# Performance work log

Hardware: AMD Instinct MI355X
Metric: run time of the kernel (lower is better)

Reference implementation:

```python
import jax, jax.numpy as jnp
import numpy as np

N_NODES = 50000
N_EDGES = 800000
IN_DIM, HID_DIM, OUT_DIM = 128, 64, 64
NEG_SLOPE = 0.2


def setup_inputs() -> dict:
    key = jax.random.key(0)
    ks = jax.random.split(key, 9)
    return {
        "x": jax.random.normal(ks[0], (N_NODES, IN_DIM), dtype=jnp.float32),
        "edge_index": jax.random.randint(ks[1], (2, N_EDGES), 0, N_NODES, dtype=jnp.int64),
        "W1": jax.random.normal(ks[2], (IN_DIM, HID_DIM), dtype=jnp.float32) * 0.1,
        "a1_src": jax.random.normal(ks[3], (HID_DIM,), dtype=jnp.float32) * 0.1,
        "a1_dst": jax.random.normal(ks[4], (HID_DIM,), dtype=jnp.float32) * 0.1,
        "b1": jnp.zeros((HID_DIM,), dtype=jnp.float32),
        "W2": jax.random.normal(ks[5], (HID_DIM, OUT_DIM), dtype=jnp.float32) * 0.1,
        "a2_src": jax.random.normal(ks[6], (OUT_DIM,), dtype=jnp.float32) * 0.1,
        "a2_dst": jax.random.normal(ks[7], (OUT_DIM,), dtype=jnp.float32) * 0.1,
        "b2": jnp.zeros((OUT_DIM,), dtype=jnp.float32),
    }


def gat_conv(x, src, dst, W, a_src, a_dst, b, n_nodes):
    """Single-head GATConv (PyG semantics, self-loops already appended)."""
    h = x @ W                               # [N, D]
    s_src = h @ a_src                       # [N]
    s_dst = h @ a_dst                       # [N]
    e = s_src[src] + s_dst[dst]             # [E] edge logits
    e = jnp.where(e >= 0, e, NEG_SLOPE * e)  # leaky_relu(0.2)
    # softmax over incoming edges of each destination node (numerically stable)
    m = jax.ops.segment_max(e, dst, num_segments=n_nodes)   # [N]
    e = jnp.exp(e - m[dst])
    denom = jax.ops.segment_sum(e, dst, num_segments=n_nodes)
    alpha = e / denom[dst]                  # [E]
    out = jax.ops.segment_sum(alpha[:, None] * h[src], dst, num_segments=n_nodes)
    return out + b


def reference(x, edge_index, W1, a1_src, a1_dst, b1, W2, a2_src, a2_dst, b2):
    n = x.shape[0]
    loop = jnp.arange(n, dtype=edge_index.dtype)
    src = jnp.concatenate([edge_index[0], loop])  # add self loops (PyG default)
    dst = jnp.concatenate([edge_index[1], loop])
    h = jax.nn.relu(gat_conv(x, src, dst, W1, a1_src, a1_dst, b1, n))
    out = gat_conv(h, src, dst, W2, a2_src, a2_dst, b2, n)
    return out
```

## Files before the change

### kernel.cpp

```cpp
#include <hip/hip_runtime.h>
#include <hip/hip_fp16.h>

#define N_NODES 50000
#define N_EDGES 800000
#define NEG_SLOPE 0.2f
#define NBKT 196
#define EBLK 200
#define CHUNK 4000

__device__ __forceinline__ float leaky(float x) { return x >= 0.f ? x : NEG_SLOPE * x; }
__device__ __forceinline__ float readlane_f(float v, int i) {
    return __uint_as_float(__builtin_amdgcn_readlane(__float_as_uint(v), i));
}
__device__ __forceinline__ unsigned enc_f(float f) {
    unsigned u = __float_as_uint(f);
    return (int)u < 0 ? ~u : (u | 0x80000000u);
}
__device__ __forceinline__ float dec_f(unsigned e) {
    return __uint_as_float((int)e < 0 ? (e & 0x7FFFFFFFu) : ~e);
}

template <int K>
__global__ __launch_bounds__(256) void gat_gemm_kernel(
    const float* __restrict__ x, const float* __restrict__ W,
    const float* __restrict__ a_src, const float* __restrict__ a_dst,
    __half* __restrict__ h, float* __restrict__ s_src, float* __restrict__ s_dst,
    unsigned* __restrict__ gmax_enc, int n)
{
    constexpr int BK = 32;
    __shared__ float Wl[BK][64];
    __shared__ float xt[BK][68];
    __shared__ float asl[64], adl[64];
    __shared__ float wm[4];

    int tid = threadIdx.x;
    if (tid < 64) { asl[tid] = a_src[tid]; adl[tid] = a_dst[tid]; }
    int tx = tid & 15, ty = tid >> 4;
    int row0 = blockIdx.x * 64;

    float acc[4][4] = {};

    for (int k0 = 0; k0 < K; k0 += BK) {
        __syncthreads();
        {
            const float4* Wg = (const float4*)&W[(size_t)k0 * 64];
            float4* Ws = (float4*)&Wl[0][0];
            Ws[tid]       = Wg[tid];
            Ws[tid + 256] = Wg[tid + 256];
        }
        #pragma unroll
        for (int it = 0; it < 2; ++it) {
            int idx = tid + it * 256;
            int r = idx >> 3, kq = idx & 7;
            int grow = row0 + r;
            float4 v = (grow < n) ? *(const float4*)&x[(size_t)grow * K + k0 + kq * 4]
                                  : make_float4(0.f, 0.f, 0.f, 0.f);
            xt[kq * 4 + 0][r] = v.x;
            xt[kq * 4 + 1][r] = v.y;
            xt[kq * 4 + 2][r] = v.z;
            xt[kq * 4 + 3][r] = v.w;
        }
        __syncthreads();

        #pragma unroll
        for (int kk = 0; kk < BK; ++kk) {
            float4 wv = *(const float4*)&Wl[kk][tx * 4];
            float4 xv = *(const float4*)&xt[kk][ty * 4];
            acc[0][0] += xv.x * wv.x; acc[0][1] += xv.x * wv.y; acc[0][2] += xv.x * wv.z; acc[0][3] += xv.x * wv.w;
            acc[1][0] += xv.y * wv.x; acc[1][1] += xv.y * wv.y; acc[1][2] += xv.y * wv.z; acc[1][3] += xv.y * wv.w;
            acc[2][0] += xv.z * wv.x; acc[2][1] += xv.z * wv.y; acc[2][2] += xv.z * wv.z; acc[2][3] += xv.z * wv.w;
            acc[3][0] += xv.w * wv.x; acc[3][1] += xv.w * wv.y; acc[3][2] += xv.w * wv.z; acc[3][3] += xv.w * wv.w;
        }
    }

    float wmax = -INFINITY;
    #pragma unroll
    for (int i = 0; i < 4; ++i) {
        int grow = row0 + ty * 4 + i;
        if (grow < n) {
            __half2 p0 = __floats2half2_rn(acc[i][0], acc[i][1]);
            __half2 p1 = __floats2half2_rn(acc[i][2], acc[i][3]);
            uint2 pk = make_uint2(*(unsigned*)&p0, *(unsigned*)&p1);
            *(uint2*)&h[(size_t)grow * 64 + tx * 4] = pk;
        }
        float s1 = acc[i][0] * asl[tx*4+0] + acc[i][1] * asl[tx*4+1]
                 + acc[i][2] * asl[tx*4+2] + acc[i][3] * asl[tx*4+3];
        float s2 = acc[i][0] * adl[tx*4+0] + acc[i][1] * adl[tx*4+1]
                 + acc[i][2] * adl[tx*4+2] + acc[i][3] * adl[tx*4+3];
        #pragma unroll
        for (int m = 1; m < 16; m <<= 1) {
            s1 += __shfl_xor(s1, m, 64);
            s2 += __shfl_xor(s2, m, 64);
        }
        if (grow < n) wmax = fmaxf(wmax, s1);
        if (tx == 0 && grow < n) { s_src[grow] = s1; s_dst[grow] = s2; }
    }
    wmax = fmaxf(wmax, __shfl_xor(wmax, 16, 64));
    wmax = fmaxf(wmax, __shfl_xor(wmax, 32, 64));
    if ((tid & 63) == 0) wm[tid >> 6] = wmax;
    __syncthreads();
    if (tid == 0) {
        float bm = fmaxf(fmaxf(wm[0], wm[1]), fmaxf(wm[2], wm[3]));
        atomicMax(gmax_enc, enc_f(bm));
    }
}

__global__ __launch_bounds__(256) void p1_count(
    const int* __restrict__ dst, int* __restrict__ cnt, unsigned* __restrict__ gmaxu)
{
    __shared__ int bins[NBKT];
    int tid = threadIdx.x, b = blockIdx.x;
    if (tid < NBKT) bins[tid] = 0;
    if (b == 0 && tid >= 254) gmaxu[tid - 254] = 0;
    __syncthreads();
    int e0 = b * CHUNK;
    for (int e = e0 + tid; e < e0 + CHUNK; e += 256)
        atomicAdd(&bins[dst[e] >> 8], 1);
    __syncthreads();
    if (tid < NBKT) cnt[b * NBKT + tid] = bins[tid];
}

__global__ __launch_bounds__(256) void p2_scan(
    int* __restrict__ cnt, int* __restrict__ btot)
{
    __shared__ int tmp[256];
    int j = blockIdx.x, tid = threadIdx.x;
    int v = (tid < EBLK) ? cnt[tid * NBKT + j] : 0;
    tmp[tid] = v; __syncthreads();
    for (int off = 1; off < 256; off <<= 1) {
        int a = (tid >= off) ? tmp[tid - off] : 0;
        __syncthreads();
        tmp[tid] += a;
        __syncthreads();
    }
    if (tid < EBLK) cnt[tid * NBKT + j] = tmp[tid] - v;
    if (tid == EBLK - 1) btot[j] = tmp[tid];
}

__global__ __launch_bounds__(256) void p3_bucket(
    const int* __restrict__ src, const int* __restrict__ dst,
    const int* __restrict__ cnt, const int* __restrict__ btot,
    unsigned* __restrict__ bkted)
{
    __shared__ int tmp[256];
    __shared__ int boffL[NBKT];
    int b = blockIdx.x, tid = threadIdx.x;
    int v = (tid < NBKT) ? btot[tid] : 0;
    tmp[tid] = v; __syncthreads();
    for (int off = 1; off < 256; off <<= 1) {
        int a = (tid >= off) ? tmp[tid - off] : 0;
        __syncthreads();
        tmp[tid] += a;
        __syncthreads();
    }
    if (tid < NBKT) boffL[tid] = (tmp[tid] - v) + cnt[b * NBKT + tid];
    __syncthreads();
    int e0 = b * CHUNK;
    for (int e = e0 + tid; e < e0 + CHUNK; e += 256) {
        int d = dst[e], s = src[e];
        int pos = atomicAdd(&boffL[d >> 8], 1);
        bkted[pos] = ((unsigned)(d & 255) << 16) | (unsigned)s;
    }
}

__global__ __launch_bounds__(256) void p4_csr(
    const unsigned* __restrict__ bkted, const int* __restrict__ btot,
    int* __restrict__ row_off, int* __restrict__ csr_src)
{
    __shared__ int tmp[256];
    __shared__ int cur[256];
    __shared__ int s_beg, s_end;
    int j = blockIdx.x, tid = threadIdx.x;
    int v = (tid < NBKT) ? btot[tid] : 0;
    tmp[tid] = v; __syncthreads();
    for (int off = 1; off < 256; off <<= 1) {
        int a = (tid >= off) ? tmp[tid - off] : 0;
        __syncthreads();
        tmp[tid] += a;
        __syncthreads();
    }
    if (tid == j) { s_beg = tmp[tid] - v; s_end = tmp[tid]; }
    cur[tid] = 0;
    __syncthreads();
    int beg = s_beg, end = s_end;

    for (int e = beg + tid; e < end; e += 256)
        atomicAdd(&cur[bkted[e] >> 16], 1);
    __syncthreads();
    int c = cur[tid];
    tmp[tid] = c; __syncthreads();
    for (int off = 1; off < 256; off <<= 1) {
        int a = (tid >= off) ? tmp[tid - off] : 0;
        __syncthreads();
        tmp[tid] += a;
        __syncthreads();
    }
    int offx = tmp[tid] - c;
    int node = j * 256 + tid;
    if (node < N_NODES) row_off[node] = beg + offx;
    if (node == 0) row_off[N_NODES] = N_EDGES;
    __syncthreads();
    cur[tid] = offx;
    __syncthreads();
    for (int e = beg + tid; e < end; e += 256) {
        unsigned u = bkted[e];
        int pos = beg + atomicAdd(&cur[u >> 16], 1);
        csr_src[pos] = (int)(u & 0xFFFFu);
    }
}

template <bool RELU>
__global__ __launch_bounds__(256) void gat_node_kernel(
    const int* __restrict__ row_off, const int* __restrict__ csr_src,
    const float* __restrict__ s_src, const float* __restrict__ s_dst,
    const __half* __restrict__ h, const float* __restrict__ b,
    const unsigned* __restrict__ gmax_enc, float* __restrict__ out, int n)
{
    int row = blockIdx.x * 4 + (threadIdx.x >> 6);
    int lane = threadIdx.x & 63;
    if (row >= n) return;

    int beg = row_off[row], end = row_off[row + 1];
    int deg = end - beg;
    float sd = s_dst[row];
    float m = leaky(dec_f(*gmax_enc) + sd);
    float s_self = s_src[row];
    float hself = __half2float(h[(size_t)row * 64 + lane]);
    float wself = __expf(leaky(s_self + sd) - m);

    if (deg <= 32) {
        int mysrc = row;
        if (lane < deg) mysrc = csr_src[beg + lane];
        float my_s = s_src[mysrc];
        float hv[32];
        #pragma unroll
        for (int j = 0; j < 32; ++j) {
            int s = __builtin_amdgcn_readlane(mysrc, j);
            hv[j] = __half2float(h[(size_t)s * 64 + lane]);
        }
        float mylogit = (lane < deg) ? leaky(my_s + sd) : -INFINITY;
        float w64 = __expf(mylogit - m);
        float den = w64;
        #pragma unroll
        for (int off = 32; off; off >>= 1)
            den += __shfl_xor(den, off, 64);
        den += wself;

        float acc = wself * hself;
        #pragma unroll
        for (int j = 0; j < 32; ++j)
            acc += readlane_f(w64, j) * hv[j];

        float v = acc / den + b[lane];
        if (RELU) v = fmaxf(v, 0.f);
        out[(size_t)row * 64 + lane] = v;
        return;
    }

    int   mysrc   = row;
    float mylogit = -INFINITY;
    if (lane < deg) {
        mysrc = csr_src[beg + lane];
        mylogit = leaky(s_src[mysrc] + sd);
    }
    float w64 = __expf(mylogit - m);
    float den = w64;
    #pragma unroll
    for (int off = 32; off; off >>= 1)
        den += __shfl_xor(den, off, 64);
    den += wself;

    float acc = wself * hself;
    int d0 = deg < 64 ? deg : 64;
    int nb = (d0 + 15) & ~15;
    for (int i = 0; i < nb; i += 16) {
        float hv[16];
        #pragma unroll
        for (int j = 0; j < 16; ++j) {
            int s = __builtin_amdgcn_readlane(mysrc, i + j);
            hv[j] = __half2float(h[(size_t)s * 64 + lane]);
        }
        #pragma unroll
        for (int j = 0; j < 16; ++j)
            acc += readlane_f(w64, i + j) * hv[j];
    }
    for (int e = beg + 64; e < end; ++e) {
        int s = csr_src[e];
        float w = __expf(leaky(s_src[s] + sd) - m);
        den += w;
        acc += w * __half2float(h[(size_t)s * 64 + lane]);
    }

    float v = acc / den + b[lane];
    if (RELU) v = fmaxf(v, 0.f);
    out[(size_t)row * 64 + lane] = v;
}

extern "C" void kernel_launch(void* const* d_in, const int* in_sizes, int n_in,
                              void* d_out, int out_size, void* d_ws, size_t ws_size,
                              hipStream_t stream) {
    const float* x   = (const float*)d_in[0];
    const int*   ei  = (const int*)d_in[1];
    const float* W1  = (const float*)d_in[2];
    const float* a1s = (const float*)d_in[3];
    const float* a1d = (const float*)d_in[4];
    const float* b1  = (const float*)d_in[5];
    const float* W2  = (const float*)d_in[6];
    const float* a2s = (const float*)d_in[7];
    const float* a2d = (const float*)d_in[8];
    const float* b2  = (const float*)d_in[9];
    float* out = (float*)d_out;

    const int* src = ei;
    const int* dst = ei + N_EDGES;

    char* p = (char*)d_ws;
    __half* h   = (__half*)p;           p += (size_t)N_NODES * 64 * 2;
    float* ssrc = (float*)p;            p += (size_t)N_NODES * 4;
    float* sdst = (float*)p;            p += (size_t)N_NODES * 4;
    int* row_off = (int*)p;             p += (size_t)(N_NODES + 1) * 4;
    unsigned* gmaxu = (unsigned*)p;     p += 4 * 4;
    int* csr_src = (int*)p;             p += (size_t)N_EDGES * 4;
    int* cnt     = (int*)p;             p += (size_t)EBLK * NBKT * 4;
    int* btot    = (int*)p;             p += (size_t)NBKT * 4;

    unsigned* bkted = (unsigned*)h;

    dim3 blk(256);
    int gemm_blocks = (N_NODES + 63) / 64;
    int node_blocks = (N_NODES + 3) / 4;

    p1_count<<<EBLK, blk, 0, stream>>>(dst, cnt, gmaxu);
    p2_scan<<<NBKT, blk, 0, stream>>>(cnt, btot);
    p3_bucket<<<EBLK, blk, 0, stream>>>(src, dst, cnt, btot, bkted);
    p4_csr<<<NBKT, blk, 0, stream>>>(bkted, btot, row_off, csr_src);

    gat_gemm_kernel<128><<<gemm_blocks, blk, 0, stream>>>(x, W1, a1s, a1d, h, ssrc, sdst, gmaxu + 0, N_NODES);
    gat_node_kernel<true><<<node_blocks, blk, 0, stream>>>(row_off, csr_src, ssrc, sdst, h, b1, gmaxu + 0, out, N_NODES);

    gat_gemm_kernel<64><<<gemm_blocks, blk, 0, stream>>>(out, W2, a2s, a2d, h, ssrc, sdst, gmaxu + 1, N_NODES);
    gat_node_kernel<false><<<node_blocks, blk, 0, stream>>>(row_off, csr_src, ssrc, sdst, h, b2, gmaxu + 1, out, N_NODES);
}
```

Baseline: 132.2 us.

## Split features into half planes, fuse GEMM with edge counting, two-edge gather per wave

Stores the fp16 projected features as two 32-column planes and runs the aggregation kernel once per plane. Each half-wave handles alternate edges, and the two halves are combined with a shuffle. The first GEMM is fused with the edge-count pass into one launch, writing per-block maxima that the scan kernel reduces, and the bucket buffer gets its own workspace. The smaller per-plane working set should fit the gathered data better in cache, at the cost of extra node-kernel launches and re-reading the CSR and scores for each plane. The small-degree fast path is removed, and nontemporal loads and stores are used for the CSR reads and output writes.

```diff
diff --git a/kernel.cpp b/kernel.cpp
--- a/kernel.cpp
+++ b/kernel.cpp
@@ -7,6 +7,7 @@
 #define NBKT 196
 #define EBLK 200
 #define CHUNK 4000
+#define GEMM_BLOCKS 782
 
 __device__ __forceinline__ float leaky(float x) { return x >= 0.f ? x : NEG_SLOPE * x; }
 __device__ __forceinline__ float readlane_f(float v, int i) {
@@ -21,11 +22,12 @@
 }
 
 template <int K>
-__global__ __launch_bounds__(256) void gat_gemm_kernel(
+__device__ __forceinline__ void gemm_body(
     const float* __restrict__ x, const float* __restrict__ W,
     const float* __restrict__ a_src, const float* __restrict__ a_dst,
-    __half* __restrict__ h, float* __restrict__ s_src, float* __restrict__ s_dst,
-    unsigned* __restrict__ gmax_enc, int n)
+    __half* __restrict__ hA, __half* __restrict__ hB,
+    float* __restrict__ s_src, float* __restrict__ s_dst,
+    float* __restrict__ bmax, unsigned* __restrict__ gmax_enc, int n)
 {
     constexpr int BK = 32;
     __shared__ float Wl[BK][64];
@@ -81,7 +83,10 @@
             __half2 p0 = __floats2half2_rn(acc[i][0], acc[i][1]);
             __half2 p1 = __floats2half2_rn(acc[i][2], acc[i][3]);
             uint2 pk = make_uint2(*(unsigned*)&p0, *(unsigned*)&p1);
-            *(uint2*)&h[(size_t)grow * 64 + tx * 4] = pk;
+            if (tx < 8)
+                *(uint2*)&hA[(size_t)grow * 32 + tx * 4] = pk;
+            else
+                *(uint2*)&hB[(size_t)grow * 32 + (tx - 8) * 4] = pk;
         }
         float s1 = acc[i][0] * asl[tx*4+0] + acc[i][1] * asl[tx*4+1]
                  + acc[i][2] * asl[tx*4+2] + acc[i][3] * asl[tx*4+3];
@@ -101,29 +106,52 @@
     __syncthreads();
     if (tid == 0) {
         float bm = fmaxf(fmaxf(wm[0], wm[1]), fmaxf(wm[2], wm[3]));
-        atomicMax(gmax_enc, enc_f(bm));
-    }
-}
-
-__global__ __launch_bounds__(256) void p1_count(
-    const int* __restrict__ dst, int* __restrict__ cnt, unsigned* __restrict__ gmaxu)
-{
-    __shared__ int bins[NBKT];
-    int tid = threadIdx.x, b = blockIdx.x;
-    if (tid < NBKT) bins[tid] = 0;
-    if (b == 0 && tid >= 254) gmaxu[tid - 254] = 0;
-    __syncthreads();
-    int e0 = b * CHUNK;
-    for (int e = e0 + tid; e < e0 + CHUNK; e += 256)
-        atomicAdd(&bins[dst[e] >> 8], 1);
-    __syncthreads();
-    if (tid < NBKT) cnt[b * NBKT + tid] = bins[tid];
+        if (bmax) bmax[blockIdx.x] = bm;
+        else      atomicMax(gmax_enc, enc_f(bm));
+    }
+}
+
+template <int K>
+__global__ __launch_bounds__(256) void fused_gemm_p1(
+    const float* __restrict__ x, const float* __restrict__ W,
+    const float* __restrict__ a_src, const float* __restrict__ a_dst,
+    __half* __restrict__ hA, __half* __restrict__ hB,
+    float* __restrict__ s_src, float* __restrict__ s_dst,
+    float* __restrict__ bmax,
+    const int* __restrict__ dst_, int* __restrict__ cnt, int n)
+{
+    if (blockIdx.x >= GEMM_BLOCKS) {
+        __shared__ int bins[NBKT];
+        int tid = threadIdx.x, b = blockIdx.x - GEMM_BLOCKS;
+        if (tid < NBKT) bins[tid] = 0;
+        __syncthreads();
+        int e0 = b * CHUNK;
+        for (int e = e0 + tid; e < e0 + CHUNK; e += 256)
+            atomicAdd(&bins[dst_[e] >> 8], 1);
+        __syncthreads();
+        if (tid < NBKT) cnt[b * NBKT + tid] = bins[tid];
+        return;
+    }
+    gemm_body<K>(x, W, a_src, a_dst, hA, hB, s_src, s_dst, bmax, nullptr, n);
+}
+
+template <int K>
+__global__ __launch_bounds__(256) void gat_gemm_kernel(
+    const float* __restrict__ x, const float* __restrict__ W,
+    const float* __restrict__ a_src, const float* __restrict__ a_dst,
+    __half* __restrict__ hA, __half* __restrict__ hB,
+    float* __restrict__ s_src, float* __restrict__ s_dst,
+    unsigned* __restrict__ gmax_enc, int n)
+{
+    gemm_body<K>(x, W, a_src, a_dst, hA, hB, s_src, s_dst, nullptr, gmax_enc, n);
 }
 
 __global__ __launch_bounds__(256) void p2_scan(
-    int* __restrict__ cnt, int* __restrict__ btot)
+    int* __restrict__ cnt, int* __restrict__ btot,
+    const float* __restrict__ bmax, unsigned* __restrict__ gmaxu)
 {
     __shared__ int tmp[256];
+    __shared__ float fm[4];
     int j = blockIdx.x, tid = threadIdx.x;
     int v = (tid < EBLK) ? cnt[tid * NBKT + j] : 0;
     tmp[tid] = v; __syncthreads();
@@ -135,6 +163,19 @@
     }
     if (tid < EBLK) cnt[tid * NBKT + j] = tmp[tid] - v;
     if (tid == EBLK - 1) btot[j] = tmp[tid];
+
+    if (j == 0) {
+        float m = -INFINITY;
+        for (int i = tid; i < GEMM_BLOCKS; i += 256) m = fmaxf(m, bmax[i]);
+        #pragma unroll
+        for (int off = 32; off; off >>= 1) m = fmaxf(m, __shfl_xor(m, off, 64));
+        if ((tid & 63) == 0) fm[tid >> 6] = m;
+        __syncthreads();
+        if (tid == 0) {
+            gmaxu[0] = enc_f(fmaxf(fmaxf(fm[0], fm[1]), fmaxf(fm[2], fm[3])));
+            gmaxu[1] = 0;
+        }
+    }
 }
 
 __global__ __launch_bounds__(256) void p3_bucket(
@@ -209,58 +250,31 @@
     }
 }
 
-template <bool RELU>
+template <bool RELU, int PLANE>
 __global__ __launch_bounds__(256) void gat_node_kernel(
     const int* __restrict__ row_off, const int* __restrict__ csr_src,
     const float* __restrict__ s_src, const float* __restrict__ s_dst,
-    const __half* __restrict__ h, const float* __restrict__ b,
+    const __half* __restrict__ hp, const float* __restrict__ b,
     const unsigned* __restrict__ gmax_enc, float* __restrict__ out, int n)
 {
     int row = blockIdx.x * 4 + (threadIdx.x >> 6);
     int lane = threadIdx.x & 63;
     if (row >= n) return;
+    int es = lane >> 5;
+    int d  = lane & 31;
 
     int beg = row_off[row], end = row_off[row + 1];
     int deg = end - beg;
     float sd = s_dst[row];
     float m = leaky(dec_f(*gmax_enc) + sd);
     float s_self = s_src[row];
-    float hself = __half2float(h[(size_t)row * 64 + lane]);
+    float hself = __half2float(hp[(size_t)row * 32 + d]);
     float wself = __expf(leaky(s_self + sd) - m);
-
-    if (deg <= 32) {
-        int mysrc = row;
-        if (lane < deg) mysrc = csr_src[beg + lane];
-        float my_s = s_src[mysrc];
-        float hv[32];
-        #pragma unroll
-        for (int j = 0; j < 32; ++j) {
-            int s = __builtin_amdgcn_readlane(mysrc, j);
-            hv[j] = __half2float(h[(size_t)s * 64 + lane]);
-        }
-        float mylogit = (lane < deg) ? leaky(my_s + sd) : -INFINITY;
-        float w64 = __expf(mylogit - m);
-        float den = w64;
-        #pragma unroll
-        for (int off = 32; off; off >>= 1)
-            den += __shfl_xor(den, off, 64);
-        den += wself;
-
-        float acc = wself * hself;
-        #pragma unroll
-        for (int j = 0; j < 32; ++j)
-            acc += readlane_f(w64, j) * hv[j];
-
-        float v = acc / den + b[lane];
-        if (RELU) v = fmaxf(v, 0.f);
-        out[(size_t)row * 64 + lane] = v;
-        return;
-    }
 
     int   mysrc   = row;
     float mylogit = -INFINITY;
     if (lane < deg) {
-        mysrc = csr_src[beg + lane];
+        mysrc = __builtin_nontemporal_load(&csr_src[beg + lane]);
         mylogit = leaky(s_src[mysrc] + sd);
     }
     float w64 = __expf(mylogit - m);
@@ -270,30 +284,39 @@
         den += __shfl_xor(den, off, 64);
     den += wself;
 
-    float acc = wself * hself;
+    float acc = (es == 0) ? wself * hself : 0.f;
+
     int d0 = deg < 64 ? deg : 64;
-    int nb = (d0 + 15) & ~15;
-    for (int i = 0; i < nb; i += 16) {
+    for (int base = 0; base < d0; base += 32) {
         float hv[16];
         #pragma unroll
         for (int j = 0; j < 16; ++j) {
-            int s = __builtin_amdgcn_readlane(mysrc, i + j);
-            hv[j] = __half2float(h[(size_t)s * 64 + lane]);
-        }
-        #pragma unroll
-        for (int j = 0; j < 16; ++j)
-            acc += readlane_f(w64, i + j) * hv[j];
+            int s0 = __builtin_amdgcn_readlane(mysrc, base + 2 * j);
+            int s1 = __builtin_amdgcn_readlane(mysrc, base + 2 * j + 1);
+            int s = es ? s1 : s0;
+            hv[j] = __half2float(hp[(size_t)s * 32 + d]);
+        }
+        #pragma unroll
+        for (int j = 0; j < 16; ++j) {
+            float w0 = readlane_f(w64, base + 2 * j);
+            float w1 = readlane_f(w64, base + 2 * j + 1);
+            acc += (es ? w1 : w0) * hv[j];
+        }
     }
     for (int e = beg + 64; e < end; ++e) {
-        int s = csr_src[e];
+        int s = __builtin_nontemporal_load(&csr_src[e]);
         float w = __expf(leaky(s_src[s] + sd) - m);
         den += w;
-        acc += w * __half2float(h[(size_t)s * 64 + lane]);
-    }
-
-    float v = acc / den + b[lane];
-    if (RELU) v = fmaxf(v, 0.f);
-    out[(size_t)row * 64 + lane] = v;
+        if (es == 0) acc += w * __half2float(hp[(size_t)s * 32 + d]);
+    }
+
+    acc += __shfl_xor(acc, 32, 64);
+
+    if (es == 0) {
+        float v = acc / den + b[PLANE * 32 + d];
+        if (RELU) v = fmaxf(v, 0.f);
+        __builtin_nontemporal_store(v, &out[(size_t)row * 64 + PLANE * 32 + d]);
+    }
 }
 
 extern "C" void kernel_launch(void* const* d_in, const int* in_sizes, int n_in,
@@ -315,29 +338,36 @@
     const int* dst = ei + N_EDGES;
 
     char* p = (char*)d_ws;
-    __half* h   = (__half*)p;           p += (size_t)N_NODES * 64 * 2;
+    __half* hA  = (__half*)p;           p += (size_t)N_NODES * 32 * 2;
+    __half* hB  = (__half*)p;           p += (size_t)N_NODES * 32 * 2;
     float* ssrc = (float*)p;            p += (size_t)N_NODES * 4;
     float* sdst = (float*)p;            p += (size_t)N_NODES * 4;
     int* row_off = (int*)p;             p += (size_t)(N_NODES + 1) * 4;
     unsigned* gmaxu = (unsigned*)p;     p += 4 * 4;
+    float* bmax = (float*)p;            p += 1024 * 4;
     int* csr_src = (int*)p;             p += (size_t)N_EDGES * 4;
     int* cnt     = (int*)p;             p += (size_t)EBLK * NBKT * 4;
     int* btot    = (int*)p;             p += (size_t)NBKT * 4;
-
-    unsigned* bkted = (unsigned*)h;
+    unsigned* bkted = (unsigned*)p;     p += (size_t)N_EDGES * 4;
 
     dim3 blk(256);
-    int gemm_blocks = (N_NODES + 63) / 64;
     int node_blocks = (N_NODES + 3) / 4;
 
-    p1_count<<<EBLK, blk, 0, stream>>>(dst, cnt, gmaxu);
-    p2_scan<<<NBKT, blk, 0, stream>>>(cnt, btot);
+    fused_gemm_p1<128><<<GEMM_BLOCKS + EBLK, blk, 0, stream>>>(
+        x, W1, a1s, a1d, hA, hB, ssrc, sdst, bmax, dst, cnt, N_NODES);
+    p2_scan<<<NBKT, blk, 0, stream>>>(cnt, btot, bmax, gmaxu);
     p3_bucket<<<EBLK, blk, 0, stream>>>(src, dst, cnt, btot, bkted);
     p4_csr<<<NBKT, blk, 0, stream>>>(bkted, btot, row_off, csr_src);
 
-    gat_gemm_kernel<128><<<gemm_blocks, blk, 0, stream>>>(x, W1, a1s, a1d, h, ssrc, sdst, gmaxu + 0, N_NODES);
-    gat_node_kernel<true><<<node_blocks, blk, 0, stream>>>(row_off, csr_src, ssrc, sdst, h, b1, gmaxu + 0, out, N_NODES);
-
-    gat_gemm_kernel<64><<<gemm_blocks, blk, 0, stream>>>(out, W2, a2s, a2d, h, ssrc, sdst, gmaxu + 1, N_NODES);
-    gat_node_kernel<false><<<node_blocks, blk, 0, stream>>>(row_off, csr_src, ssrc, sdst, h, b2, gmaxu + 1, out, N_NODES);
-}
+    gat_node_kernel<true, 0><<<node_blocks, blk, 0, stream>>>(
+        row_off, csr_src, ssrc, sdst, hA, b1, gmaxu + 0, out, N_NODES);
+    gat_node_kernel<true, 1><<<node_blocks, blk, 0, stream>>>(
+        row_off, csr_src, ssrc, sdst, hB, b1, gmaxu + 0, out, N_NODES);
+
+    gat_gemm_kernel<64><<<GEMM_BLOCKS, blk, 0, stream>>>(
+        out, W2, a2s, a2d, hA, hB, ssrc, sdst, gmaxu + 1, N_NODES);
+    gat_node_kernel<false, 0><<<node_blocks, blk, 0, stream>>>(
+        row_off, csr_src, ssrc, sdst, hA, b2, gmaxu + 1, out, N_NODES);
+    gat_node_kernel<false, 1><<<node_blocks, blk, 0, stream>>>(
+        row_off, csr_src, ssrc, sdst, hB, b2, gmaxu + 1, out, N_NODES);
+}
```

New measurement: 203.7 us. 1.54x slower.

## Gather neighbor features as 4-wide half vectors across wavefront quarters

Applied to the files above, without the earlier changes.

Restructures the node aggregation kernel so each wavefront splits into four 16-lane quarters. Each lane loads 4 half values (8 bytes) of a neighbor row per gather, so four edges are processed in parallel, and the partial sums are reduced with cross-quarter shuffles before one quarter writes a float4. The aim is fewer, wider memory transactions and fewer serialized readlane steps per edge. In exchange it adds shuffle reductions, a more complex high-degree path that recomputes the denominator, and idle lanes during the final write.

```diff
diff --git a/kernel.cpp b/kernel.cpp
--- a/kernel.cpp
+++ b/kernel.cpp
@@ -9,9 +9,6 @@
 #define CHUNK 4000
 
 __device__ __forceinline__ float leaky(float x) { return x >= 0.f ? x : NEG_SLOPE * x; }
-__device__ __forceinline__ float readlane_f(float v, int i) {
-    return __uint_as_float(__builtin_amdgcn_readlane(__float_as_uint(v), i));
-}
 __device__ __forceinline__ unsigned enc_f(float f) {
     unsigned u = __float_as_uint(f);
     return (int)u < 0 ? ~u : (u | 0x80000000u);
@@ -219,43 +216,14 @@
     int row = blockIdx.x * 4 + (threadIdx.x >> 6);
     int lane = threadIdx.x & 63;
     if (row >= n) return;
+    int q = lane >> 4;
+    int t = lane & 15;
 
     int beg = row_off[row], end = row_off[row + 1];
     int deg = end - beg;
     float sd = s_dst[row];
     float m = leaky(dec_f(*gmax_enc) + sd);
-    float s_self = s_src[row];
-    float hself = __half2float(h[(size_t)row * 64 + lane]);
-    float wself = __expf(leaky(s_self + sd) - m);
-
-    if (deg <= 32) {
-        int mysrc = row;
-        if (lane < deg) mysrc = csr_src[beg + lane];
-        float my_s = s_src[mysrc];
-        float hv[32];
-        #pragma unroll
-        for (int j = 0; j < 32; ++j) {
-            int s = __builtin_amdgcn_readlane(mysrc, j);
-            hv[j] = __half2float(h[(size_t)s * 64 + lane]);
-        }
-        float mylogit = (lane < deg) ? leaky(my_s + sd) : -INFINITY;
-        float w64 = __expf(mylogit - m);
-        float den = w64;
-        #pragma unroll
-        for (int off = 32; off; off >>= 1)
-            den += __shfl_xor(den, off, 64);
-        den += wself;
-
-        float acc = wself * hself;
-        #pragma unroll
-        for (int j = 0; j < 32; ++j)
-            acc += readlane_f(w64, j) * hv[j];
-
-        float v = acc / den + b[lane];
-        if (RELU) v = fmaxf(v, 0.f);
-        out[(size_t)row * 64 + lane] = v;
-        return;
-    }
+    float wself = __expf(leaky(s_src[row] + sd) - m);
 
     int   mysrc   = row;
     float mylogit = -INFINITY;
@@ -270,30 +238,76 @@
         den += __shfl_xor(den, off, 64);
     den += wself;
 
-    float acc = wself * hself;
-    int d0 = deg < 64 ? deg : 64;
-    int nb = (d0 + 15) & ~15;
-    for (int i = 0; i < nb; i += 16) {
-        float hv[16];
+    float4 acc = make_float4(0.f, 0.f, 0.f, 0.f);
+
+    if (deg <= 64) {
+        for (int base = 0; base < deg; base += 32) {
+            uint2 hv[8]; float wj[8];
+            #pragma unroll
+            for (int j = 0; j < 8; ++j) {
+                int idx = base + 4 * j + q;
+                int   s = __shfl(mysrc, idx, 64);
+                wj[j]   = __shfl(w64,   idx, 64);
+                hv[j] = *(const uint2*)&h[(size_t)s * 64 + 4 * t];
+            }
+            #pragma unroll
+            for (int j = 0; j < 8; ++j) {
+                float2 lo = __half22float2(*(__half2*)&hv[j].x);
+                float2 hi = __half22float2(*(__half2*)&hv[j].y);
+                acc.x += wj[j] * lo.x; acc.y += wj[j] * lo.y;
+                acc.z += wj[j] * hi.x; acc.w += wj[j] * hi.y;
+            }
+        }
+    } else {
+        int nb = (deg + 31) & ~31;
+        for (int base = 0; base < nb; base += 32) {
+            uint2 hv[8]; float wj[8];
+            #pragma unroll
+            for (int j = 0; j < 8; ++j) {
+                int idx = base + 4 * j + q;
+                int e = beg + idx;
+                int s = (idx < deg) ? csr_src[e] : row;
+                float w = (idx < deg) ? __expf(leaky(s_src[s] + sd) - m) : 0.f;
+                if (idx >= 64 && idx < deg) den += w / 64.f;
+                wj[j] = w;
+                hv[j] = *(const uint2*)&h[(size_t)s * 64 + 4 * t];
+            }
+            #pragma unroll
+            for (int j = 0; j < 8; ++j) {
+                float2 lo = __half22float2(*(__half2*)&hv[j].x);
+                float2 hi = __half22float2(*(__half2*)&hv[j].y);
+                acc.x += wj[j] * lo.x; acc.y += wj[j] * lo.y;
+                acc.z += wj[j] * hi.x; acc.w += wj[j] * hi.y;
+            }
+        }
+        den = wself;
+        for (int e = beg + lane; e < end; e += 64)
+            den += __expf(leaky(s_src[csr_src[e]] + sd) - m);
         #pragma unroll
-        for (int j = 0; j < 16; ++j) {
-            int s = __builtin_amdgcn_readlane(mysrc, i + j);
-            hv[j] = __half2float(h[(size_t)s * 64 + lane]);
-        }
-        #pragma unroll
-        for (int j = 0; j < 16; ++j)
-            acc += readlane_f(w64, i + j) * hv[j];
-    }
-    for (int e = beg + 64; e < end; ++e) {
-        int s = csr_src[e];
-        float w = __expf(leaky(s_src[s] + sd) - m);
-        den += w;
-        acc += w * __half2float(h[(size_t)s * 64 + lane]);
-    }
-
-    float v = acc / den + b[lane];
-    if (RELU) v = fmaxf(v, 0.f);
-    out[(size_t)row * 64 + lane] = v;
+        for (int off = 32; off; off >>= 1)
+            den += __shfl_xor(den, off, 64);
+    }
+
+    acc.x += __shfl_xor(acc.x, 16, 64); acc.x += __shfl_xor(acc.x, 32, 64);
+    acc.y += __shfl_xor(acc.y, 16, 64); acc.y += __shfl_xor(acc.y, 32, 64);
+    acc.z += __shfl_xor(acc.z, 16, 64); acc.z += __shfl_xor(acc.z, 32, 64);
+    acc.w += __shfl_xor(acc.w, 16, 64); acc.w += __shfl_xor(acc.w, 32, 64);
+
+    if (q == 0) {
+        uint2 hs = *(const uint2*)&h[(size_t)row * 64 + 4 * t];
+        float2 lo = __half22float2(*(__half2*)&hs.x);
+        float2 hi = __half22float2(*(__half2*)&hs.y);
+        float4 v;
+        v.x = (acc.x + wself * lo.x) / den + b[4*t+0];
+        v.y = (acc.y + wself * lo.y) / den + b[4*t+1];
+        v.z = (acc.z + wself * hi.x) / den + b[4*t+2];
+        v.w = (acc.w + wself * hi.y) / den + b[4*t+3];
+        if (RELU) {
+            v.x = fmaxf(v.x, 0.f); v.y = fmaxf(v.y, 0.f);
+            v.z = fmaxf(v.z, 0.f); v.w = fmaxf(v.w, 0.f);
+        }
+        *(float4*)&out[(size_t)row * 64 + 4 * t] = v;
+    }
 }
 
 extern "C" void kernel_launch(void* const* d_in, const int* in_sizes, int n_in,
```

Result: slower. 147.5 us (+11.6%).

## Fuse layer-1 GEMM with edge counting and merge CSR build stages via grid barriers

Applied to the files above, without the earlier changes.

Runs the first GEMM and the destination-bucket counting in one launch, and merges the scan, bucketing and CSR passes into a single persistent kernel that uses software grid barriers. The global max for layer 1 becomes a per-block max array reduced inside the fused kernel instead of an atomic. The aim is fewer kernel launches and fewer gaps between dependent stages. The bucket buffer now gets its own workspace region instead of aliasing h. The grid barrier relies on all 200 blocks being resident at once, and the barrier counters are reset in the previous kernel.

```diff
diff --git a/kernel.cpp b/kernel.cpp
--- a/kernel.cpp
+++ b/kernel.cpp
@@ -7,6 +7,7 @@
 #define NBKT 196
 #define EBLK 200
 #define CHUNK 4000
+#define GEMM_BLOCKS 782
 
 __device__ __forceinline__ float leaky(float x) { return x >= 0.f ? x : NEG_SLOPE * x; }
 __device__ __forceinline__ float readlane_f(float v, int i) {
@@ -20,12 +21,24 @@
     return __uint_as_float((int)e < 0 ? (e & 0x7FFFFFFFu) : ~e);
 }
 
+__device__ __forceinline__ void grid_barrier(unsigned* ctr, int grid) {
+    __syncthreads();
+    if (threadIdx.x == 0) {
+        __threadfence();
+        __hip_atomic_fetch_add(ctr, 1u, __ATOMIC_ACQ_REL, __HIP_MEMORY_SCOPE_AGENT);
+        while (__hip_atomic_load(ctr, __ATOMIC_ACQUIRE, __HIP_MEMORY_SCOPE_AGENT) < (unsigned)grid)
+            __builtin_amdgcn_s_sleep(2);
+        __threadfence();
+    }
+    __syncthreads();
+}
+
 template <int K>
-__global__ __launch_bounds__(256) void gat_gemm_kernel(
+__device__ __forceinline__ void gemm_body(
     const float* __restrict__ x, const float* __restrict__ W,
     const float* __restrict__ a_src, const float* __restrict__ a_dst,
     __half* __restrict__ h, float* __restrict__ s_src, float* __restrict__ s_dst,
-    unsigned* __restrict__ gmax_enc, int n)
+    float* __restrict__ bmax, unsigned* __restrict__ gmax_enc, int n)
 {
     constexpr int BK = 32;
     __shared__ float Wl[BK][64];
@@ -101,111 +114,146 @@
     __syncthreads();
     if (tid == 0) {
         float bm = fmaxf(fmaxf(wm[0], wm[1]), fmaxf(wm[2], wm[3]));
-        atomicMax(gmax_enc, enc_f(bm));
-    }
-}
-
-__global__ __launch_bounds__(256) void p1_count(
-    const int* __restrict__ dst, int* __restrict__ cnt, unsigned* __restrict__ gmaxu)
-{
-    __shared__ int bins[NBKT];
-    int tid = threadIdx.x, b = blockIdx.x;
-    if (tid < NBKT) bins[tid] = 0;
-    if (b == 0 && tid >= 254) gmaxu[tid - 254] = 0;
-    __syncthreads();
-    int e0 = b * CHUNK;
-    for (int e = e0 + tid; e < e0 + CHUNK; e += 256)
-        atomicAdd(&bins[dst[e] >> 8], 1);
-    __syncthreads();
-    if (tid < NBKT) cnt[b * NBKT + tid] = bins[tid];
-}
-
-__global__ __launch_bounds__(256) void p2_scan(
-    int* __restrict__ cnt, int* __restrict__ btot)
+        if (bmax) bmax[blockIdx.x] = bm;
+        else      atomicMax(gmax_enc, enc_f(bm));
+    }
+}
+
+template <int K>
+__global__ __launch_bounds__(256) void fused_gemm_p1(
+    const float* __restrict__ x, const float* __restrict__ W,
+    const float* __restrict__ a_src, const float* __restrict__ a_dst,
+    __half* __restrict__ h, float* __restrict__ s_src, float* __restrict__ s_dst,
+    float* __restrict__ bmax,
+    const int* __restrict__ dst_, int* __restrict__ cnt,
+    unsigned* __restrict__ gmaxu, int n)
+{
+    if (blockIdx.x >= GEMM_BLOCKS) {
+        __shared__ int bins[NBKT];
+        int tid = threadIdx.x, b = blockIdx.x - GEMM_BLOCKS;
+        if (tid < NBKT) bins[tid] = 0;
+        if (b == 0 && tid >= 253) gmaxu[tid - 252] = 0;
+        __syncthreads();
+        int e0 = b * CHUNK;
+        for (int e = e0 + tid; e < e0 + CHUNK; e += 256)
+            atomicAdd(&bins[dst_[e] >> 8], 1);
+        __syncthreads();
+        if (tid < NBKT) cnt[b * NBKT + tid] = bins[tid];
+        return;
+    }
+    gemm_body<K>(x, W, a_src, a_dst, h, s_src, s_dst, bmax, nullptr, n);
+}
+
+template <int K>
+__global__ __launch_bounds__(256) void gat_gemm_kernel(
+    const float* __restrict__ x, const float* __restrict__ W,
+    const float* __restrict__ a_src, const float* __restrict__ a_dst,
+    __half* __restrict__ h, float* __restrict__ s_src, float* __restrict__ s_dst,
+    unsigned* __restrict__ gmax_enc, int n)
+{
+    gemm_body<K>(x, W, a_src, a_dst, h, s_src, s_dst, nullptr, gmax_enc, n);
+}
+
+__global__ __launch_bounds__(256) void p234_fused(
+    int* __restrict__ cnt, int* __restrict__ btot,
+    const float* __restrict__ bmax, unsigned* __restrict__ gmaxu,
+    const int* __restrict__ src, const int* __restrict__ dst,
+    unsigned* __restrict__ bkted,
+    int* __restrict__ row_off, int* __restrict__ csr_src)
 {
     __shared__ int tmp[256];
-    int j = blockIdx.x, tid = threadIdx.x;
-    int v = (tid < EBLK) ? cnt[tid * NBKT + j] : 0;
-    tmp[tid] = v; __syncthreads();
-    for (int off = 1; off < 256; off <<= 1) {
-        int a = (tid >= off) ? tmp[tid - off] : 0;
-        __syncthreads();
-        tmp[tid] += a;
-        __syncthreads();
-    }
-    if (tid < EBLK) cnt[tid * NBKT + j] = tmp[tid] - v;
-    if (tid == EBLK - 1) btot[j] = tmp[tid];
-}
-
-__global__ __launch_bounds__(256) void p3_bucket(
-    const int* __restrict__ src, const int* __restrict__ dst,
-    const int* __restrict__ cnt, const int* __restrict__ btot,
-    unsigned* __restrict__ bkted)
-{
-    __shared__ int tmp[256];
-    __shared__ int boffL[NBKT];
+    __shared__ int aux[256];
+    __shared__ int s_beg, s_end;
+    __shared__ float fm[4];
     int b = blockIdx.x, tid = threadIdx.x;
-    int v = (tid < NBKT) ? btot[tid] : 0;
-    tmp[tid] = v; __syncthreads();
-    for (int off = 1; off < 256; off <<= 1) {
-        int a = (tid >= off) ? tmp[tid - off] : 0;
-        __syncthreads();
-        tmp[tid] += a;
-        __syncthreads();
-    }
-    if (tid < NBKT) boffL[tid] = (tmp[tid] - v) + cnt[b * NBKT + tid];
-    __syncthreads();
-    int e0 = b * CHUNK;
-    for (int e = e0 + tid; e < e0 + CHUNK; e += 256) {
-        int d = dst[e], s = src[e];
-        int pos = atomicAdd(&boffL[d >> 8], 1);
-        bkted[pos] = ((unsigned)(d & 255) << 16) | (unsigned)s;
-    }
-}
-
-__global__ __launch_bounds__(256) void p4_csr(
-    const unsigned* __restrict__ bkted, const int* __restrict__ btot,
-    int* __restrict__ row_off, int* __restrict__ csr_src)
-{
-    __shared__ int tmp[256];
-    __shared__ int cur[256];
-    __shared__ int s_beg, s_end;
-    int j = blockIdx.x, tid = threadIdx.x;
-    int v = (tid < NBKT) ? btot[tid] : 0;
-    tmp[tid] = v; __syncthreads();
-    for (int off = 1; off < 256; off <<= 1) {
-        int a = (tid >= off) ? tmp[tid - off] : 0;
-        __syncthreads();
-        tmp[tid] += a;
-        __syncthreads();
-    }
-    if (tid == j) { s_beg = tmp[tid] - v; s_end = tmp[tid]; }
-    cur[tid] = 0;
-    __syncthreads();
-    int beg = s_beg, end = s_end;
-
-    for (int e = beg + tid; e < end; e += 256)
-        atomicAdd(&cur[bkted[e] >> 16], 1);
-    __syncthreads();
-    int c = cur[tid];
-    tmp[tid] = c; __syncthreads();
-    for (int off = 1; off < 256; off <<= 1) {
-        int a = (tid >= off) ? tmp[tid - off] : 0;
-        __syncthreads();
-        tmp[tid] += a;
-        __syncthreads();
-    }
-    int offx = tmp[tid] - c;
-    int node = j * 256 + tid;
-    if (node < N_NODES) row_off[node] = beg + offx;
-    if (node == 0) row_off[N_NODES] = N_EDGES;
-    __syncthreads();
-    cur[tid] = offx;
-    __syncthreads();
-    for (int e = beg + tid; e < end; e += 256) {
-        unsigned u = bkted[e];
-        int pos = beg + atomicAdd(&cur[u >> 16], 1);
-        csr_src[pos] = (int)(u & 0xFFFFu);
+
+    if (b < NBKT) {
+        int j = b;
+        int v = (tid < EBLK) ? cnt[tid * NBKT + j] : 0;
+        tmp[tid] = v; __syncthreads();
+        for (int off = 1; off < 256; off <<= 1) {
+            int a = (tid >= off) ? tmp[tid - off] : 0;
+            __syncthreads();
+            tmp[tid] += a;
+            __syncthreads();
+        }
+        if (tid < EBLK) cnt[tid * NBKT + j] = tmp[tid] - v;
+        if (tid == EBLK - 1) btot[j] = tmp[tid];
+    }
+    if (b == 0) {
+        __syncthreads();
+        float m = -INFINITY;
+        for (int i = tid; i < GEMM_BLOCKS; i += 256) m = fmaxf(m, bmax[i]);
+        #pragma unroll
+        for (int off = 32; off; off >>= 1) m = fmaxf(m, __shfl_xor(m, off, 64));
+        if ((tid & 63) == 0) fm[tid >> 6] = m;
+        __syncthreads();
+        if (tid == 0)
+            gmaxu[0] = enc_f(fmaxf(fmaxf(fm[0], fm[1]), fmaxf(fm[2], fm[3])));
+    }
+
+    grid_barrier(&gmaxu[2], EBLK);
+
+    {
+        int v = (tid < NBKT) ? btot[tid] : 0;
+        tmp[tid] = v; __syncthreads();
+        for (int off = 1; off < 256; off <<= 1) {
+            int a = (tid >= off) ? tmp[tid - off] : 0;
+            __syncthreads();
+            tmp[tid] += a;
+            __syncthreads();
+        }
+        if (tid < NBKT) aux[tid] = (tmp[tid] - v) + cnt[b * NBKT + tid];
+        __syncthreads();
+        int e0 = b * CHUNK;
+        for (int e = e0 + tid; e < e0 + CHUNK; e += 256) {
+            int d = dst[e], s = src[e];
+            int pos = atomicAdd(&aux[d >> 8], 1);
+            bkted[pos] = ((unsigned)(d & 255) << 16) | (unsigned)s;
+        }
+    }
+
+    grid_barrier(&gmaxu[3], EBLK);
+
+    if (b >= NBKT) return;
+    {
+        int j = b;
+        int v = (tid < NBKT) ? btot[tid] : 0;
+        tmp[tid] = v; __syncthreads();
+        for (int off = 1; off < 256; off <<= 1) {
+            int a = (tid >= off) ? tmp[tid - off] : 0;
+            __syncthreads();
+            tmp[tid] += a;
+            __syncthreads();
+        }
+        if (tid == j) { s_beg = tmp[tid] - v; s_end = tmp[tid]; }
+        aux[tid] = 0;
+        __syncthreads();
+        int beg = s_beg, end = s_end;
+
+        for (int e = beg + tid; e < end; e += 256)
+            atomicAdd(&aux[bkted[e] >> 16], 1);
+        __syncthreads();
+        int c = aux[tid];
+        tmp[tid] = c; __syncthreads();
+        for (int off = 1; off < 256; off <<= 1) {
+            int a = (tid >= off) ? tmp[tid - off] : 0;
+            __syncthreads();
+            tmp[tid] += a;
+            __syncthreads();
+        }
+        int offx = tmp[tid] - c;
+        int node = j * 256 + tid;
+        if (node < N_NODES) row_off[node] = beg + offx;
+        if (node == 0) row_off[N_NODES] = N_EDGES;
+        __syncthreads();
+        aux[tid] = offx;
+        __syncthreads();
+        for (int e = beg + tid; e < end; e += 256) {
+            unsigned u = bkted[e];
+            int pos = beg + atomicAdd(&aux[u >> 16], 1);
+            csr_src[pos] = (int)(u & 0xFFFFu);
+        }
     }
 }
 
@@ -320,24 +368,23 @@
     float* sdst = (float*)p;            p += (size_t)N_NODES * 4;
     int* row_off = (int*)p;             p += (size_t)(N_NODES + 1) * 4;
     unsigned* gmaxu = (unsigned*)p;     p += 4 * 4;
+    float* bmax = (float*)p;            p += 1024 * 4;
     int* csr_src = (int*)p;             p += (size_t)N_EDGES * 4;
     int* cnt     = (int*)p;             p += (size_t)EBLK * NBKT * 4;
     int* btot    = (int*)p;             p += (size_t)NBKT * 4;
-
-    unsigned* bkted = (unsigned*)h;
+    unsigned* bkted = (unsigned*)p;     p += (size_t)N_EDGES * 4;
 
     dim3 blk(256);
-    int gemm_blocks = (N_NODES + 63) / 64;
     int node_blocks = (N_NODES + 3) / 4;
 
-    p1_count<<<EBLK, blk, 0, stream>>>(dst, cnt, gmaxu);
-    p2_scan<<<NBKT, blk, 0, stream>>>(cnt, btot);
-    p3_bucket<<<EBLK, blk, 0, stream>>>(src, dst, cnt, btot, bkted);
-    p4_csr<<<NBKT, blk, 0, stream>>>(bkted, btot, row_off, csr_src);
-
-    gat_gemm_kernel<128><<<gemm_blocks, blk, 0, stream>>>(x, W1, a1s, a1d, h, ssrc, sdst, gmaxu + 0, N_NODES);
-    gat_node_kernel<true><<<node_blocks, blk, 0, stream>>>(row_off, csr_src, ssrc, sdst, h, b1, gmaxu + 0, out, N_NODES);
-
-    gat_gemm_kernel<64><<<gemm_blocks, blk, 0, stream>>>(out, W2, a2s, a2d, h, ssrc, sdst, gmaxu + 1, N_NODES);
-    gat_node_kernel<false><<<node_blocks, blk, 0, stream>>>(row_off, csr_src, ssrc, sdst, h, b2, gmaxu + 1, out, N_NODES);
-}
+    fused_gemm_p1<128><<<GEMM_BLOCKS + EBLK, blk, 0, stream>>>(
+        x, W1, a1s, a1d, h, ssrc, sdst, bmax, dst, cnt, gmaxu, N_NODES);
+    p234_fused<<<EBLK, blk, 0, stream>>>(
+        cnt, btot, bmax, gmaxu, src, dst, bkted, row_off, csr_src);
+    gat_node_kernel<true><<<node_blocks, blk, 0, stream>>>(
+        row_off, csr_src, ssrc, sdst, h, b1, gmaxu + 0, out, N_NODES);
+    gat_gemm_kernel<64><<<GEMM_BLOCKS, blk, 0, stream>>>(
+        out, W2, a2s, a2d, h, ssrc, sdst, gmaxu + 1, N_NODES);
+    gat_node_kernel<false><<<node_blocks, blk, 0, stream>>>(
+        row_off, csr_src, ssrc, sdst, h, b2, gmaxu + 1, out, N_NODES);
+}
```

Measured after the change: 163.1 us. +23.4%, slower.
